# Optimization experiments

Measured on AMD Instinct MI355X. Metric: run time of the kernel, lower is better.

The kernel has to match this reference:

```python
import jax, jax.numpy as jnp
import numpy as np

B, N, H = 2048, 5, 5
IN, HID, OUT = 7, 2048, 512  # IN = 1 + c + c^2 with c = (H-1)//2 = 2


def setup_inputs() -> dict:
    key = jax.random.key(0)
    ks = jax.random.split(key, 7)
    k_in = 1.0 / np.sqrt(IN).astype(np.float32)
    k_h = 1.0 / np.sqrt(HID).astype(np.float32)
    return {
        "ins": jax.random.normal(ks[0], (B, N, H, H), jnp.float32),
        "w1": (jax.random.uniform(ks[1], (4, HID, IN), jnp.float32) - 0.5) * k_in,
        "b1": (jax.random.uniform(ks[2], (HID,), jnp.float32) - 0.5) * k_in,
        "w2": (jax.random.uniform(ks[3], (4, HID, HID), jnp.float32) - 0.5) * k_h,
        "b2": (jax.random.uniform(ks[4], (HID,), jnp.float32) - 0.5) * k_h,
        "w3": (jax.random.uniform(ks[5], (4, OUT, HID), jnp.float32) - 0.5) * k_h,
        "b3": (jax.random.uniform(ks[6], (OUT,), jnp.float32) - 0.5) * k_h,
        "ln_g": jnp.ones((HID,), jnp.float32),
        "ln_b": jnp.zeros((HID,), jnp.float32),
    }


def _rot90(x):
    # matches torch: x.flip(3).permute(0,1,3,2)
    return jnp.swapaxes(jnp.flip(x, axis=3), 2, 3)


def _orbit_stack(x):
    b, n = x.shape[0], x.shape[1]
    c = (x.shape[-1] - 1) // 2  # = 2 for H=5
    center = x[:, :, c, c]  # (B,N)
    parts = []
    xi = x
    for _ in range(4):  # fixed C4 group orbit, not a data loop
        parts.append(xi[:, :, :c, :c + 1].reshape(b, n, -1))  # (B,N,c+c^2)
        xi = _rot90(xi)
    orb = jnp.stack(parts, axis=-1)  # (B,N,c+c^2,4)
    cen = jnp.broadcast_to(center[..., None, None], (b, n, 1, 4))
    out = jnp.concatenate([cen, orb], axis=2)  # (B,N,n_orbits,4)
    return jnp.transpose(out, (0, 1, 3, 2))  # (B,N,4,n_orbits)


def _c4conv(w, bias, x):
    # block-circulant kernel: mat[g,h] = w[(h-g) % 4]
    mat = jnp.stack([jnp.roll(w, i, axis=0) for i in range(4)], axis=0)  # (4,4,out,in)
    return jnp.einsum('ghij,bnhj->bngi', mat, x) + bias


def _layernorm(x, g, b, eps=1e-5):
    m = jnp.mean(x, axis=-1, keepdims=True)
    v = jnp.mean(jnp.square(x - m), axis=-1, keepdims=True)
    return (x - m) / jnp.sqrt(v + eps) * g + b


def reference(ins, w1, b1, w2, b2, w3, b3, ln_g, ln_b):
    h = _orbit_stack(ins)                          # (B,N,4,7)
    h = jax.nn.relu(_c4conv(w1, b1, h))            # (B,N,4,HID)
    h = jax.nn.relu(_layernorm(_c4conv(w2, b2, h), ln_g, ln_b))
    return _c4conv(w3, b3, h)                      # (B,N,4,OUT)
```

## Files before the change

### kernel.cpp

```cpp
#include <hip/hip_runtime.h>
#include <stdint.h>


#define HID 2048
#define MROWS 10240

typedef float floatx4 __attribute__((ext_vector_type(4)));
typedef __bf16 bf16x8 __attribute__((ext_vector_type(8)));

__device__ __forceinline__ unsigned short f2bf(float f) {
  union { float f; unsigned int u; } v; v.f = f;
  unsigned int r = v.u + 0x7fffu + ((v.u >> 16) & 1u);
  return (unsigned short)(r >> 16);
}
__device__ __forceinline__ float bf2f(unsigned short s) {
  union { unsigned int u; float f; } v; v.u = ((unsigned int)s) << 16;
  return v.f;
}

template <int NO>
__global__ __launch_bounds__(256) void wtrans_kernel(const float* __restrict__ w,
                                                     unsigned short* __restrict__ W0s,
                                                     unsigned short* __restrict__ W2s,
                                                     unsigned short* __restrict__ Bc) {
  int idx = blockIdx.x * 256 + threadIdx.x;
  int i = idx >> 9, j4 = idx & 511;
  const float4* wp = (const float4*)w;
  float4 w0 = wp[0 * NO * 512 + i * 512 + j4];
  float4 w1 = wp[1 * NO * 512 + i * 512 + j4];
  float4 w2 = wp[2 * NO * 512 + i * 512 + j4];
  float4 w3 = wp[3 * NO * 512 + i * 512 + j4];
  ushort4 s0, s2, vr, vi, nvi;
#define DO(c)                                        \
  s0.c = f2bf(w0.c + w1.c + w2.c + w3.c);            \
  s2.c = f2bf(w0.c - w1.c + w2.c - w3.c);            \
  vr.c = f2bf(w0.c - w2.c);                          \
  vi.c = f2bf(w1.c - w3.c);                          \
  nvi.c = f2bf(-(w1.c - w3.c));
  DO(x) DO(y) DO(z) DO(w)
#undef DO
  ((ushort4*)W0s)[i * 512 + j4] = s0;
  ((ushort4*)W2s)[i * 512 + j4] = s2;
  ((ushort4*)Bc)[i * 1024 + j4] = vr;
  ((ushort4*)Bc)[i * 1024 + 512 + j4] = nvi;
  ((ushort4*)Bc)[(NO + i) * 1024 + j4] = vi;
  ((ushort4*)Bc)[(NO + i) * 1024 + 512 + j4] = vr;
}

__global__ __launch_bounds__(256) void layer1_kernel(const float* __restrict__ ins,
                                                     const float* __restrict__ w1,
                                                     const float* __restrict__ b1,
                                                     unsigned short* __restrict__ h1s,
                                                     int row0) {
  __shared__ float orbs[32][28];
  int t = threadIdx.x;
  int b0 = blockIdx.x * 32;
  int i = blockIdx.y * 256 + t;
  if (t < 32) {
    const float* x = ins + (size_t)(row0 + b0 + t) * 25;
    float v[25];
#pragma unroll
    for (int p = 0; p < 25; ++p) v[p] = x[p];
    float* o = orbs[t];
    o[0] = v[12]; o[7] = v[12]; o[14] = v[12]; o[21] = v[12];
#pragma unroll
    for (int r = 0; r < 2; ++r)
#pragma unroll
      for (int c = 0; c < 3; ++c) {
        int m = 1 + r * 3 + c;
        o[m]      = v[r * 5 + c];
        o[7 + m]  = v[c * 5 + (4 - r)];
        o[14 + m] = v[(4 - r) * 5 + (4 - c)];
        o[21 + m] = v[(4 - c) * 5 + r];
      }
  }
  __syncthreads();
  float w[4][7];
#pragma unroll
  for (int r = 0; r < 4; ++r)
#pragma unroll
    for (int j = 0; j < 7; ++j) w[r][j] = w1[(r * HID + i) * 7 + j];
  float bias = b1[i];
  for (int s = 0; s < 32; ++s) {
    float a[4] = {bias, bias, bias, bias};
#pragma unroll
    for (int hh = 0; hh < 4; ++hh)
#pragma unroll
      for (int j = 0; j < 7; ++j) {
        float ov = orbs[s][hh * 7 + j];
#pragma unroll
        for (int g = 0; g < 4; ++g) a[g] += w[(hh - g) & 3][j] * ov;
      }
    float h0 = fmaxf(a[0], 0.f), h1 = fmaxf(a[1], 0.f);
    float h2 = fmaxf(a[2], 0.f), h3 = fmaxf(a[3], 0.f);
    size_t base = (size_t)(b0 + s) * 8192 + i;
    h1s[base]        = f2bf(h0 + h1 + h2 + h3);
    h1s[base + 2048] = f2bf(h0 - h1 + h2 - h3);
    h1s[base + 4096] = f2bf(h0 - h2);
    h1s[base + 6144] = f2bf(h3 - h1);
  }
}

#define PW 4


__global__ __launch_bounds__(512, 2) void gemm_spec(const unsigned short* __restrict__ A,
                                                    const unsigned short* __restrict__ B0,
                                                    const unsigned short* __restrict__ B1,
                                                    const unsigned short* __restrict__ B2,
                                                    float* __restrict__ Cf,
                                                    unsigned short* __restrict__ Cb,
                                                    int s1, int s2, int nhalf, int N0, int ldc) {
  __shared__ __align__(16) unsigned short As[2][16384];
  __shared__ __align__(16) unsigned short Bs[2][16384];
  int tid = threadIdx.x;
  int wave = tid >> 6, lane = tid & 63;
  int lane15 = lane & 15, lane4 = lane >> 4, l7 = lane15 & 7;
  int wm = wave >> 2, wn = wave & 3;
  int wm64 = wm << 6, wn32 = wn << 5;

  int nwg = gridDim.x * gridDim.y;
  int q8 = nwg >> 3;
  int flat = blockIdx.y * gridDim.x + blockIdx.x;
  int swz = (flat & 7) * q8 + (flat >> 3);
  int pgy = PW * gridDim.y;
  int panel = swz / pgy, rem = swz % pgy;
  int mt = rem / PW;
  int wnt = panel * PW + (rem % PW);
  int pp = wnt >> 2, pj = wnt & 3;
  int nt = (pj < 2) ? (nhalf + 2 * pp + pj) : (2 * pp + (pj - 2));
  int m0 = mt * 256;

  const unsigned short* Bp;
  int K, aoff, coff, nloc;
  if (nt < s1)      { Bp = B0; K = 2048; aoff = 0;    coff = 0;      nloc = nt * 256; }
  else if (nt < s2) { Bp = B1; K = 2048; aoff = 2048; coff = N0;     nloc = (nt - s1) * 256; }
  else              { Bp = B2; K = 4096; aoff = 4096; coff = 2 * N0; nloc = (nt - s2) * 256; }
  int ldb = K;

  int srow = tid >> 3;
  int scol = ((tid & 7) ^ ((tid >> 3) & 7)) << 3;
  const unsigned short* Agb = A + (size_t)(m0 + srow) * 8192 + aoff + scol;
  const unsigned short* Bgb = Bp + (size_t)(nloc + (srow & 31)) * ldb + scol;
  int bs64 = (srow >> 5) << 6;

#define STA(buf, mh, kk)                                                                              \
  __builtin_amdgcn_global_load_lds(                                                                   \
      (const __attribute__((address_space(1))) void*)(Agb + (size_t)((mh) * 64) * 8192 + (kk)),       \
      (__attribute__((address_space(3))) void*)((char*)As[buf] + (mh) * 16384 + wave * 1024),         \
      16, 0, 0);                                                                                      \
  __builtin_amdgcn_global_load_lds(                                                                   \
      (const __attribute__((address_space(1))) void*)(Agb + (size_t)((mh) * 64 + 128) * 8192 + (kk)), \
      (__attribute__((address_space(3))) void*)((char*)As[buf] + (mh) * 16384 + 8192 + wave * 1024),  \
      16, 0, 0)

#define STB(buf, nh, kk)                                                                              \
  __builtin_amdgcn_global_load_lds(                                                                   \
      (const __attribute__((address_space(1))) void*)(Bgb + (size_t)(bs64 + (nh) * 32) * ldb + (kk)), \
      (__attribute__((address_space(3))) void*)((char*)Bs[buf] + (nh) * 16384 + wave * 1024),         \
      16, 0, 0);                                                                                      \
  __builtin_amdgcn_global_load_lds(                                                                   \
      (const __attribute__((address_space(1))) void*)(Bgb + (size_t)(bs64 + 128 + (nh) * 32) * ldb + (kk)), \
      (__attribute__((address_space(3))) void*)((char*)Bs[buf] + (nh) * 16384 + 8192 + wave * 1024),  \
      16, 0, 0)

#define RAF(buf, mh)                                                                                  \
  _Pragma("unroll") for (int mi_ = 0; mi_ < 4; ++mi_)                                                 \
  _Pragma("unroll") for (int ks_ = 0; ks_ < 2; ++ks_)                                                 \
      af[mi_][ks_] = *(const bf16x8*)((const char*)As[buf] +                                          \
          (((mh) * 128 + wm64 + mi_ * 16 + lane15) << 7) + (((ks_ * 4 + lane4) ^ l7) << 4))

#define RBF(dst, buf, nh)                                                                             \
  _Pragma("unroll") for (int ni_ = 0; ni_ < 2; ++ni_)                                                 \
  _Pragma("unroll") for (int ks_ = 0; ks_ < 2; ++ks_)                                                 \
      dst[ni_][ks_] = *(const bf16x8*)((const char*)Bs[buf] +                                         \
          (((nh) * 128 + wn32 + ni_ * 16 + lane15) << 7) + (((ks_ * 4 + lane4) ^ l7) << 4))

#define MM(mh, nh, bF)                                                                                \
  _Pragma("unroll") for (int mi_ = 0; mi_ < 4; ++mi_)                                                 \
  _Pragma("unroll") for (int ni_ = 0; ni_ < 2; ++ni_)                                                 \
  _Pragma("unroll") for (int ks_ = 0; ks_ < 2; ++ks_)                                                 \
      acc[(mh) * 4 + mi_][(nh) * 2 + ni_] = __builtin_amdgcn_mfma_f32_16x16x32_bf16(                  \
          af[mi_][ks_], bF[ni_][ks_], acc[(mh) * 4 + mi_][(nh) * 2 + ni_], 0, 0, 0)

#define BAR() __builtin_amdgcn_s_barrier()
#define LGKM0() asm volatile("s_waitcnt lgkmcnt(0)" ::: "memory")
#define LGKM8() asm volatile("s_waitcnt lgkmcnt(8)" ::: "memory")
#define VM6() asm volatile("s_waitcnt vmcnt(6)" ::: "memory")

  bf16x8 af[4][2], b0r[2][2], b1r[2][2];
  const floatx4 fz = {0.f, 0.f, 0.f, 0.f};
  floatx4 acc[8][4];
#pragma unroll
  for (int a = 0; a < 8; ++a)
#pragma unroll
    for (int b = 0; b < 4; ++b) acc[a][b] = fz;

  STA(0, 0, 0); STB(0, 0, 0); STB(0, 1, 0); STA(0, 1, 0);
  STA(1, 0, 64); STB(1, 0, 64); STB(1, 1, 64);
  VM6();
  BAR();

  for (int k0 = 0; k0 < K; k0 += 128) {
    RAF(0, 0); RBF(b0r, 0, 0);
    STA(1, 1, k0 + 64);
    LGKM8();
    BAR(); LGKM0();
    __builtin_amdgcn_s_setprio(1); MM(0, 0, b0r); __builtin_amdgcn_s_setprio(0);
    BAR();
    RBF(b1r, 0, 1);
    STA(0, 0, k0 + 128);
    BAR(); LGKM0();
    __builtin_amdgcn_s_setprio(1); MM(0, 1, b1r); __builtin_amdgcn_s_setprio(0);
    BAR();
    RAF(0, 1);
    STB(0, 0, k0 + 128);
    BAR(); LGKM0();
    __builtin_amdgcn_s_setprio(1); MM(1, 0, b0r); __builtin_amdgcn_s_setprio(0);
    BAR();
    STB(0, 1, k0 + 128);
    BAR(); LGKM0();
    __builtin_amdgcn_s_setprio(1); MM(1, 1, b1r); __builtin_amdgcn_s_setprio(0);
    VM6();
    BAR();
    RAF(1, 0); RBF(b0r, 1, 0);
    STA(0, 1, k0 + 128);
    LGKM8();
    BAR(); LGKM0();
    __builtin_amdgcn_s_setprio(1); MM(0, 0, b0r); __builtin_amdgcn_s_setprio(0);
    BAR();
    RBF(b1r, 1, 1);
    STA(1, 0, k0 + 192);
    BAR(); LGKM0();
    __builtin_amdgcn_s_setprio(1); MM(0, 1, b1r); __builtin_amdgcn_s_setprio(0);
    BAR();
    RAF(1, 1);
    STB(1, 0, k0 + 192);
    BAR(); LGKM0();
    __builtin_amdgcn_s_setprio(1); MM(1, 0, b0r); __builtin_amdgcn_s_setprio(0);
    BAR();
    STB(1, 1, k0 + 192);
    BAR(); LGKM0();
    __builtin_amdgcn_s_setprio(1); MM(1, 1, b1r); __builtin_amdgcn_s_setprio(0);
    VM6();
    BAR();
  }
  asm volatile("s_waitcnt vmcnt(0)" ::: "memory");

#pragma unroll
  for (int ni = 0; ni < 4; ++ni) {
    int col = coff + nloc + wn * 64 + (ni >> 1) * 32 + (ni & 1) * 16 + lane15;
#pragma unroll
    for (int mi = 0; mi < 8; ++mi) {
      int row = m0 + wm * 128 + (mi >> 2) * 64 + (mi & 3) * 16 + lane4 * 4;
      if (Cb) {
#pragma unroll
        for (int r = 0; r < 4; ++r)
          Cb[(size_t)(row + r) * ldc + col] = f2bf(acc[mi][ni][r]);
      } else {
#pragma unroll
        for (int r = 0; r < 4; ++r)
          Cf[(size_t)(row + r) * ldc + col] = acc[mi][ni][r];
      }
    }
  }
#undef STA
#undef STB
#undef RAF
#undef RBF
#undef MM
#undef BAR
#undef LGKM0
#undef LGKM8
#undef VM6
}

__global__ __launch_bounds__(256) void ln_spec_kernel(const unsigned short* __restrict__ C2,
                                                      const float* __restrict__ b2,
                                                      const float* __restrict__ ln_g,
                                                      const float* __restrict__ ln_b,
                                                      unsigned short* __restrict__ h1s) {
  int t = threadIdx.x;
  size_t base = (size_t)blockIdx.x * 8192;
  const ushort4* p = (const ushort4*)(C2 + base);
  const float4* bp2 = (const float4*)b2;
  float4 y[4][2];
  float s[4] = {0, 0, 0, 0}, q[4] = {0, 0, 0, 0};
#pragma unroll
  for (int hl = 0; hl < 2; ++hl) {
    int j = hl * 256 + t;
    ushort4 u0 = p[j], u2 = p[512 + j], ur = p[1024 + j], ui = p[1536 + j];
    float4 bb = bp2[j];
#define DO(c)                                                   \
  {                                                             \
    float v0 = bf2f(u0.c), v2 = bf2f(u2.c);                     \
    float vr = bf2f(ur.c), vi = bf2f(ui.c);                     \
    float e0 = 0.25f * (v0 + v2 + 2.f * vr) + bb.c;             \
    float e1 = 0.25f * (v0 - v2 - 2.f * vi) + bb.c;             \
    float e2 = 0.25f * (v0 + v2 - 2.f * vr) + bb.c;             \
    float e3 = 0.25f * (v0 - v2 + 2.f * vi) + bb.c;             \
    y[0][hl].c = e0; y[1][hl].c = e1; y[2][hl].c = e2; y[3][hl].c = e3; \
    s[0] += e0; q[0] += e0 * e0; s[1] += e1; q[1] += e1 * e1;   \
    s[2] += e2; q[2] += e2 * e2; s[3] += e3; q[3] += e3 * e3;   \
  }
    DO(x) DO(y) DO(z) DO(w)
#undef DO
  }
#pragma unroll
  for (int off = 32; off > 0; off >>= 1)
#pragma unroll
    for (int g = 0; g < 4; ++g) {
      s[g] += __shfl_down(s[g], off, 64);
      q[g] += __shfl_down(q[g], off, 64);
    }
  __shared__ float rs[4][4], rq[4][4];
  int w = t >> 6, l = t & 63;
  if (l == 0)
#pragma unroll
    for (int g = 0; g < 4; ++g) { rs[w][g] = s[g]; rq[w][g] = q[g]; }
  __syncthreads();
  float mean[4], rstd[4];
#pragma unroll
  for (int g = 0; g < 4; ++g) {
    float ss = rs[0][g] + rs[1][g] + rs[2][g] + rs[3][g];
    float qq = rq[0][g] + rq[1][g] + rq[2][g] + rq[3][g];
    mean[g] = ss * (1.f / HID);
    float var = qq * (1.f / HID) - mean[g] * mean[g];
    rstd[g] = rsqrtf(var + 1e-5f);
  }
  const float4* gp = (const float4*)ln_g;
  const float4* lbp = (const float4*)ln_b;
#pragma unroll
  for (int hl = 0; hl < 2; ++hl) {
    int j = hl * 256 + t;
    float4 gg = gp[j], lb = lbp[j];
    ushort4 o[4];
#define DO(c)                                                               \
  {                                                                         \
    float h0 = fmaxf((y[0][hl].c - mean[0]) * rstd[0] * gg.c + lb.c, 0.f);  \
    float h1 = fmaxf((y[1][hl].c - mean[1]) * rstd[1] * gg.c + lb.c, 0.f);  \
    float h2 = fmaxf((y[2][hl].c - mean[2]) * rstd[2] * gg.c + lb.c, 0.f);  \
    float h3 = fmaxf((y[3][hl].c - mean[3]) * rstd[3] * gg.c + lb.c, 0.f);  \
    o[0].c = f2bf(h0 + h1 + h2 + h3);                                       \
    o[1].c = f2bf(h0 - h1 + h2 - h3);                                       \
    o[2].c = f2bf(h0 - h2);                                                 \
    o[3].c = f2bf(h3 - h1);                                                 \
  }
    DO(x) DO(y) DO(z) DO(w)
#undef DO
    size_t ob = (size_t)blockIdx.x * 8192;
#pragma unroll
    for (int pl = 0; pl < 4; ++pl)
      ((ushort4*)(h1s + ob + pl * 2048))[j] = o[pl];
  }
}

__global__ __launch_bounds__(256) void out_ep_kernel(const float* __restrict__ Z,
                                                     const float* __restrict__ b3,
                                                     float* __restrict__ out) {
  int e = blockIdx.x * 256 + threadIdx.x;
  int row = e >> 9, i = e & 511;
  size_t base = (size_t)row * 2048;
  float z0 = Z[base + i], z2 = Z[base + 512 + i];
  float zr = Z[base + 1024 + i], zi = Z[base + 1536 + i];
  float bv = b3[i];
  out[base + i]        = 0.25f * (z0 + z2 + 2.f * zr) + bv;
  out[base + 512 + i]  = 0.25f * (z0 - z2 - 2.f * zi) + bv;
  out[base + 1024 + i] = 0.25f * (z0 + z2 - 2.f * zr) + bv;
  out[base + 1536 + i] = 0.25f * (z0 - z2 + 2.f * zi) + bv;
}

extern "C" void kernel_launch(void* const* d_in, const int* in_sizes, int n_in,
                              void* d_out, int out_size, void* d_ws, size_t ws_size,
                              hipStream_t stream) {
  const float* ins = (const float*)d_in[0];
  const float* w1  = (const float*)d_in[1];
  const float* b1  = (const float*)d_in[2];
  const float* w2  = (const float*)d_in[3];
  const float* b2  = (const float*)d_in[4];
  const float* w3  = (const float*)d_in[5];
  const float* b3  = (const float*)d_in[6];
  const float* lng = (const float*)d_in[7];
  const float* lnb = (const float*)d_in[8];
  float* out = (float*)d_out;
  char* ws = (char*)d_ws;

  unsigned short* W0s2 = (unsigned short*)ws;
  unsigned short* W2s2 = W0s2 + 4194304;
  unsigned short* Bc2  = W2s2 + 4194304;
  unsigned short* W0s3 = Bc2 + 16777216;
  unsigned short* W2s3 = W0s3 + 1048576;
  unsigned short* Bc3  = W2s3 + 1048576;
  const size_t WT_BYTES = 62914560ull;
  char* chunk_base = ws + WT_BYTES;

  static const int Pcand[8] = {1, 2, 4, 5, 8, 10, 20, 40};
  int P = 40;
  for (int pi = 0; pi < 8; ++pi) {
    size_t mc = (size_t)MROWS / Pcand[pi];
    size_t need = WT_BYTES + mc * 8192 * 2 * 2 + 256;
    if (need <= ws_size) { P = Pcand[pi]; break; }
  }
  const int Mc = MROWS / P;
  unsigned short* h1s = (unsigned short*)chunk_base;
  unsigned short* C2  = (unsigned short*)(chunk_base + (size_t)Mc * 8192 * 2);
  float*          Z   = (float*)C2;

  wtrans_kernel<2048><<<4096, 256, 0, stream>>>(w2, W0s2, W2s2, Bc2);
  wtrans_kernel<512><<<1024, 256, 0, stream>>>(w3, W0s3, W2s3, Bc3);

  for (int c = 0; c < P; ++c) {
    int row0 = c * Mc;
    layer1_kernel<<<dim3(Mc / 32, 8), 256, 0, stream>>>(ins, w1, b1, h1s, row0);
    gemm_spec<<<dim3(32, Mc / 256), 512, 0, stream>>>(h1s, W0s2, W2s2, Bc2, nullptr, C2,
                                                      8, 16, 16, 2048, 8192);
    ln_spec_kernel<<<Mc, 256, 0, stream>>>(C2, b2, lng, lnb, h1s);
    gemm_spec<<<dim3(8, Mc / 256), 512, 0, stream>>>(h1s, W0s3, W2s3, Bc3, Z, nullptr,
                                                     2, 4, 4, 512, 2048);
    out_ep_kernel<<<Mc * 2, 256, 0, stream>>>(Z, b3, out + (size_t)row0 * 2048);
  }
}
```

Baseline: 1.230 ms.

## Make spectral GEMM persistent with serpentine tile order and restructure chunking

The GEMM kernel becomes persistent: a fixed grid of 256 workgroups loops over output tiles in passes, ordering the long-K (K=4096) tiles first and alternating direction each pass to balance load. This replaces the old swizzled 2D grid. When the workspace is large enough, the host processes layer 2 in two halves and writes LayerNorm output in place into a full-size H2 buffer, then runs a single layer-3 GEMM over all rows, cutting launch count and small-chunk tail effects. The cost is a larger workspace and possible loss of L2 locality from the new tile ordering.

```diff
diff --git a/kernel.cpp b/kernel.cpp
--- a/kernel.cpp
+++ b/kernel.cpp
@@ -101,8 +101,6 @@
   }
 }
 
-#define PW 4
-
 
 __global__ __launch_bounds__(512, 2) void gemm_spec(const unsigned short* __restrict__ A,
                                                     const unsigned short* __restrict__ B0,
@@ -110,7 +108,8 @@
                                                     const unsigned short* __restrict__ B2,
                                                     float* __restrict__ Cf,
                                                     unsigned short* __restrict__ Cb,
-                                                    int s1, int s2, int nhalf, int N0, int ldc) {
+                                                    int s1, int s2, int N0, int ldc,
+                                                    int NT, int NTL, int MTN) {
   __shared__ __align__(16) unsigned short As[2][16384];
   __shared__ __align__(16) unsigned short Bs[2][16384];
   int tid = threadIdx.x;
@@ -119,29 +118,8 @@
   int wm = wave >> 2, wn = wave & 3;
   int wm64 = wm << 6, wn32 = wn << 5;
 
-  int nwg = gridDim.x * gridDim.y;
-  int q8 = nwg >> 3;
-  int flat = blockIdx.y * gridDim.x + blockIdx.x;
-  int swz = (flat & 7) * q8 + (flat >> 3);
-  int pgy = PW * gridDim.y;
-  int panel = swz / pgy, rem = swz % pgy;
-  int mt = rem / PW;
-  int wnt = panel * PW + (rem % PW);
-  int pp = wnt >> 2, pj = wnt & 3;
-  int nt = (pj < 2) ? (nhalf + 2 * pp + pj) : (2 * pp + (pj - 2));
-  int m0 = mt * 256;
-
-  const unsigned short* Bp;
-  int K, aoff, coff, nloc;
-  if (nt < s1)      { Bp = B0; K = 2048; aoff = 0;    coff = 0;      nloc = nt * 256; }
-  else if (nt < s2) { Bp = B1; K = 2048; aoff = 2048; coff = N0;     nloc = (nt - s1) * 256; }
-  else              { Bp = B2; K = 4096; aoff = 4096; coff = 2 * N0; nloc = (nt - s2) * 256; }
-  int ldb = K;
-
   int srow = tid >> 3;
   int scol = ((tid & 7) ^ ((tid >> 3) & 7)) << 3;
-  const unsigned short* Agb = A + (size_t)(m0 + srow) * 8192 + aoff + scol;
-  const unsigned short* Bgb = Bp + (size_t)(nloc + (srow & 31)) * ldb + scol;
   int bs64 = (srow >> 5) << 6;
 
 #define STA(buf, mh, kk)                                                                              \
@@ -191,76 +169,100 @@
   bf16x8 af[4][2], b0r[2][2], b1r[2][2];
   const floatx4 fz = {0.f, 0.f, 0.f, 0.f};
   floatx4 acc[8][4];
-#pragma unroll
-  for (int a = 0; a < 8; ++a)
-#pragma unroll
-    for (int b = 0; b < 4; ++b) acc[a][b] = fz;
-
-  STA(0, 0, 0); STB(0, 0, 0); STB(0, 1, 0); STA(0, 1, 0);
-  STA(1, 0, 64); STB(1, 0, 64); STB(1, 1, 64);
-  VM6();
-  BAR();
-
-  for (int k0 = 0; k0 < K; k0 += 128) {
-    RAF(0, 0); RBF(b0r, 0, 0);
-    STA(1, 1, k0 + 64);
-    LGKM8();
-    BAR(); LGKM0();
-    __builtin_amdgcn_s_setprio(1); MM(0, 0, b0r); __builtin_amdgcn_s_setprio(0);
-    BAR();
-    RBF(b1r, 0, 1);
-    STA(0, 0, k0 + 128);
-    BAR(); LGKM0();
-    __builtin_amdgcn_s_setprio(1); MM(0, 1, b1r); __builtin_amdgcn_s_setprio(0);
-    BAR();
-    RAF(0, 1);
-    STB(0, 0, k0 + 128);
-    BAR(); LGKM0();
-    __builtin_amdgcn_s_setprio(1); MM(1, 0, b0r); __builtin_amdgcn_s_setprio(0);
-    BAR();
-    STB(0, 1, k0 + 128);
-    BAR(); LGKM0();
-    __builtin_amdgcn_s_setprio(1); MM(1, 1, b1r); __builtin_amdgcn_s_setprio(0);
+
+  int G = (int)gridDim.x;
+  for (int pass = 0;; ++pass) {
+    int base = pass * G;
+    if (base >= NT) break;
+    int wt = (pass & 1) ? (base + G - 1 - (int)blockIdx.x) : (base + (int)blockIdx.x);
+    if (wt >= NT) continue;
+
+    int mt, nt;
+    if (wt < NTL) { int j = wt / MTN; nt = s2 + j; mt = wt - j * MTN; }
+    else          { int w2_ = wt - NTL; int j = w2_ / MTN; nt = j; mt = w2_ - j * MTN; }
+    int m0 = mt * 256;
+
+    const unsigned short* Bp;
+    int K, aoff, coff, nloc;
+    if (nt < s1)      { Bp = B0; K = 2048; aoff = 0;    coff = 0;      nloc = nt * 256; }
+    else if (nt < s2) { Bp = B1; K = 2048; aoff = 2048; coff = N0;     nloc = (nt - s1) * 256; }
+    else              { Bp = B2; K = 4096; aoff = 4096; coff = 2 * N0; nloc = (nt - s2) * 256; }
+    int ldb = K;
+
+    const unsigned short* Agb = A + (size_t)(m0 + srow) * 8192 + aoff + scol;
+    const unsigned short* Bgb = Bp + (size_t)(nloc + (srow & 31)) * ldb + scol;
+
+#pragma unroll
+    for (int a = 0; a < 8; ++a)
+#pragma unroll
+      for (int b = 0; b < 4; ++b) acc[a][b] = fz;
+
+    STA(0, 0, 0); STB(0, 0, 0); STB(0, 1, 0); STA(0, 1, 0);
+    STA(1, 0, 64); STB(1, 0, 64); STB(1, 1, 64);
     VM6();
     BAR();
-    RAF(1, 0); RBF(b0r, 1, 0);
-    STA(0, 1, k0 + 128);
-    LGKM8();
-    BAR(); LGKM0();
-    __builtin_amdgcn_s_setprio(1); MM(0, 0, b0r); __builtin_amdgcn_s_setprio(0);
-    BAR();
-    RBF(b1r, 1, 1);
-    STA(1, 0, k0 + 192);
-    BAR(); LGKM0();
-    __builtin_amdgcn_s_setprio(1); MM(0, 1, b1r); __builtin_amdgcn_s_setprio(0);
-    BAR();
-    RAF(1, 1);
-    STB(1, 0, k0 + 192);
-    BAR(); LGKM0();
-    __builtin_amdgcn_s_setprio(1); MM(1, 0, b0r); __builtin_amdgcn_s_setprio(0);
-    BAR();
-    STB(1, 1, k0 + 192);
-    BAR(); LGKM0();
-    __builtin_amdgcn_s_setprio(1); MM(1, 1, b1r); __builtin_amdgcn_s_setprio(0);
-    VM6();
-    BAR();
-  }
-  asm volatile("s_waitcnt vmcnt(0)" ::: "memory");
-
-#pragma unroll
-  for (int ni = 0; ni < 4; ++ni) {
-    int col = coff + nloc + wn * 64 + (ni >> 1) * 32 + (ni & 1) * 16 + lane15;
-#pragma unroll
-    for (int mi = 0; mi < 8; ++mi) {
-      int row = m0 + wm * 128 + (mi >> 2) * 64 + (mi & 3) * 16 + lane4 * 4;
-      if (Cb) {
-#pragma unroll
-        for (int r = 0; r < 4; ++r)
-          Cb[(size_t)(row + r) * ldc + col] = f2bf(acc[mi][ni][r]);
-      } else {
-#pragma unroll
-        for (int r = 0; r < 4; ++r)
-          Cf[(size_t)(row + r) * ldc + col] = acc[mi][ni][r];
+
+    for (int k0 = 0; k0 < K; k0 += 128) {
+      RAF(0, 0); RBF(b0r, 0, 0);
+      STA(1, 1, k0 + 64);
+      LGKM8();
+      BAR(); LGKM0();
+      __builtin_amdgcn_s_setprio(1); MM(0, 0, b0r); __builtin_amdgcn_s_setprio(0);
+      BAR();
+      RBF(b1r, 0, 1);
+      STA(0, 0, k0 + 128);
+      BAR(); LGKM0();
+      __builtin_amdgcn_s_setprio(1); MM(0, 1, b1r); __builtin_amdgcn_s_setprio(0);
+      BAR();
+      RAF(0, 1);
+      STB(0, 0, k0 + 128);
+      BAR(); LGKM0();
+      __builtin_amdgcn_s_setprio(1); MM(1, 0, b0r); __builtin_amdgcn_s_setprio(0);
+      BAR();
+      STB(0, 1, k0 + 128);
+      BAR(); LGKM0();
+      __builtin_amdgcn_s_setprio(1); MM(1, 1, b1r); __builtin_amdgcn_s_setprio(0);
+      VM6();
+      BAR();
+      RAF(1, 0); RBF(b0r, 1, 0);
+      STA(0, 1, k0 + 128);
+      LGKM8();
+      BAR(); LGKM0();
+      __builtin_amdgcn_s_setprio(1); MM(0, 0, b0r); __builtin_amdgcn_s_setprio(0);
+      BAR();
+      RBF(b1r, 1, 1);
+      STA(1, 0, k0 + 192);
+      BAR(); LGKM0();
+      __builtin_amdgcn_s_setprio(1); MM(0, 1, b1r); __builtin_amdgcn_s_setprio(0);
+      BAR();
+      RAF(1, 1);
+      STB(1, 0, k0 + 192);
+      BAR(); LGKM0();
+      __builtin_amdgcn_s_setprio(1); MM(1, 0, b0r); __builtin_amdgcn_s_setprio(0);
+      BAR();
+      STB(1, 1, k0 + 192);
+      BAR(); LGKM0();
+      __builtin_amdgcn_s_setprio(1); MM(1, 1, b1r); __builtin_amdgcn_s_setprio(0);
+      VM6();
+      BAR();
+    }
+    asm volatile("s_waitcnt vmcnt(0)" ::: "memory");
+
+#pragma unroll
+    for (int ni = 0; ni < 4; ++ni) {
+      int col = coff + nloc + wn * 64 + (ni >> 1) * 32 + (ni & 1) * 16 + lane15;
+#pragma unroll
+      for (int mi = 0; mi < 8; ++mi) {
+        int row = m0 + wm * 128 + (mi >> 2) * 64 + (mi & 3) * 16 + lane4 * 4;
+        if (Cb) {
+#pragma unroll
+          for (int r = 0; r < 4; ++r)
+            Cb[(size_t)(row + r) * ldc + col] = f2bf(acc[mi][ni][r]);
+        } else {
+#pragma unroll
+          for (int r = 0; r < 4; ++r)
+            Cf[(size_t)(row + r) * ldc + col] = acc[mi][ni][r];
+        }
       }
     }
   }
@@ -275,11 +277,11 @@
 #undef VM6
 }
 
-__global__ __launch_bounds__(256) void ln_spec_kernel(const unsigned short* __restrict__ C2,
+__global__ __launch_bounds__(256) void ln_spec_kernel(const unsigned short* C2,
                                                       const float* __restrict__ b2,
                                                       const float* __restrict__ ln_g,
                                                       const float* __restrict__ ln_b,
-                                                      unsigned short* __restrict__ h1s) {
+                                                      unsigned short* h1s) {
   int t = threadIdx.x;
   size_t base = (size_t)blockIdx.x * 8192;
   const ushort4* p = (const ushort4*)(C2 + base);
@@ -394,29 +396,53 @@
   const size_t WT_BYTES = 62914560ull;
   char* chunk_base = ws + WT_BYTES;
 
-  static const int Pcand[8] = {1, 2, 4, 5, 8, 10, 20, 40};
-  int P = 40;
-  for (int pi = 0; pi < 8; ++pi) {
-    size_t mc = (size_t)MROWS / Pcand[pi];
-    size_t need = WT_BYTES + mc * 8192 * 2 * 2 + 256;
-    if (need <= ws_size) { P = Pcand[pi]; break; }
-  }
-  const int Mc = MROWS / P;
-  unsigned short* h1s = (unsigned short*)chunk_base;
-  unsigned short* C2  = (unsigned short*)(chunk_base + (size_t)Mc * 8192 * 2);
-  float*          Z   = (float*)C2;
-
   wtrans_kernel<2048><<<4096, 256, 0, stream>>>(w2, W0s2, W2s2, Bc2);
   wtrans_kernel<512><<<1024, 256, 0, stream>>>(w3, W0s3, W2s3, Bc3);
 
-  for (int c = 0; c < P; ++c) {
-    int row0 = c * Mc;
-    layer1_kernel<<<dim3(Mc / 32, 8), 256, 0, stream>>>(ins, w1, b1, h1s, row0);
-    gemm_spec<<<dim3(32, Mc / 256), 512, 0, stream>>>(h1s, W0s2, W2s2, Bc2, nullptr, C2,
-                                                      8, 16, 16, 2048, 8192);
-    ln_spec_kernel<<<Mc, 256, 0, stream>>>(C2, b2, lng, lnb, h1s);
-    gemm_spec<<<dim3(8, Mc / 256), 512, 0, stream>>>(h1s, W0s3, W2s3, Bc3, Z, nullptr,
-                                                     2, 4, 4, 512, 2048);
-    out_ep_kernel<<<Mc * 2, 256, 0, stream>>>(Z, b3, out + (size_t)row0 * 2048);
-  }
-}
+  const size_t H1_BYTES = (size_t)5120 * 8192 * 2;
+  const size_t H2_BYTES = (size_t)MROWS * 8192 * 2;
+  const size_t need_full = WT_BYTES + H1_BYTES + H2_BYTES + 4096;
+
+  if (ws_size >= need_full) {
+    unsigned short* h1s = (unsigned short*)chunk_base;
+    float*          Z   = (float*)chunk_base;
+    unsigned short* H2  = (unsigned short*)(chunk_base + H1_BYTES);
+    const int Mc = 5120, MTN = Mc / 256;
+    for (int c = 0; c < 2; ++c) {
+      int row0 = c * Mc;
+      unsigned short* H2c = H2 + (size_t)row0 * 8192;
+      layer1_kernel<<<dim3(Mc / 32, 8), 256, 0, stream>>>(ins, w1, b1, h1s, row0);
+      gemm_spec<<<256, 512, 0, stream>>>(h1s, W0s2, W2s2, Bc2, nullptr, H2c,
+                                         8, 16, 2048, 8192, 32 * MTN, 16 * MTN, MTN);
+      ln_spec_kernel<<<Mc, 256, 0, stream>>>(H2c, b2, lng, lnb, H2c);
+    }
+    {
+      const int MT3 = MROWS / 256;
+      gemm_spec<<<256, 512, 0, stream>>>(H2, W0s3, W2s3, Bc3, Z, nullptr,
+                                         2, 4, 512, 2048, 8 * MT3, 4 * MT3, MT3);
+      out_ep_kernel<<<MROWS * 2, 256, 0, stream>>>(Z, b3, out);
+    }
+  } else {
+    static const int Pcand[8] = {1, 2, 4, 5, 8, 10, 20, 40};
+    int P = 40;
+    for (int pi = 0; pi < 8; ++pi) {
+      size_t mc = (size_t)MROWS / Pcand[pi];
+      size_t need = WT_BYTES + mc * 8192 * 2 * 2 + 4096;
+      if (need <= ws_size) { P = Pcand[pi]; break; }
+    }
+    const int Mc = MROWS / P, MTN = Mc / 256;
+    unsigned short* h1s = (unsigned short*)chunk_base;
+    unsigned short* C2  = (unsigned short*)(chunk_base + (size_t)Mc * 8192 * 2);
+    float*          Z   = (float*)C2;
+    for (int c = 0; c < P; ++c) {
+      int row0 = c * Mc;
+      layer1_kernel<<<dim3(Mc / 32, 8), 256, 0, stream>>>(ins, w1, b1, h1s, row0);
+      gemm_spec<<<256, 512, 0, stream>>>(h1s, W0s2, W2s2, Bc2, nullptr, C2,
+                                         8, 16, 2048, 8192, 32 * MTN, 16 * MTN, MTN);
+      ln_spec_kernel<<<Mc, 256, 0, stream>>>(C2, b2, lng, lnb, h1s);
+      gemm_spec<<<256, 512, 0, stream>>>(h1s, W0s3, W2s3, Bc3, Z, nullptr,
+                                         2, 4, 512, 2048, 8 * MTN, 4 * MTN, MTN);
+      out_ep_kernel<<<Mc * 2, 256, 0, stream>>>(Z, b3, out + (size_t)row0 * 2048);
+    }
+  }
+}
```

Result: faster. 1.001 ms (-18.6%).
